# Performance work log

Hardware: AMD Instinct MI355X
Metric: run time of the kernel (lower is better)

## Reference

```python
import jax, jax.numpy as jnp
import numpy as np

N, D_IN = 8192, 1024
FC1, FC2, FC3 = 256, 128, 64
DQK = FC3 // 8  # 8


def setup_inputs() -> dict:
    key = jax.random.key(0)
    ks = jax.random.split(key, 20)
    s = 0.05
    inp = {
        "x": jax.random.normal(ks[0], (N, D_IN), jnp.float32),
        # feature extractor MLP (dropout omitted: eval mode)
        "W1": jax.random.normal(ks[1], (D_IN, FC1), jnp.float32) * s,
        "b1": jnp.zeros((FC1,), jnp.float32),
        "W2": jax.random.normal(ks[2], (FC1, FC2), jnp.float32) * s,
        "b2": jnp.zeros((FC2,), jnp.float32),
        "W3": jax.random.normal(ks[3], (FC2, FC3), jnp.float32) * s,
        "b3": jnp.zeros((FC3,), jnp.float32),
        # 1x1 conv Q/K/V == linear layers on the 64-dim embedding
        "Wq": jax.random.normal(ks[4], (FC3, DQK), jnp.float32) * s,
        "bq": jnp.zeros((DQK,), jnp.float32),
        "Wk": jax.random.normal(ks[5], (FC3, DQK), jnp.float32) * s,
        "bk": jnp.zeros((DQK,), jnp.float32),
        "Wv": jax.random.normal(ks[6], (FC3, FC3), jnp.float32) * s,
        "bv": jnp.zeros((FC3,), jnp.float32),
        "gamma": jnp.array([0.5], jnp.float32),  # learned residual scale (init 0 in torch)
        # attention-pooling branch
        "Wa1": jax.random.normal(ks[7], (FC3, FC3), jnp.float32) * s,
        "ba1": jnp.zeros((FC3,), jnp.float32),
        "Wa2": jax.random.normal(ks[8], (FC3, 1), jnp.float32) * s,
        "ba2": jnp.zeros((1,), jnp.float32),
        # classifier
        "Wc": jax.random.normal(ks[9], (FC3, 1), jnp.float32) * s,
        "bc": jnp.zeros((1,), jnp.float32),
    }
    return inp


def reference(x, W1, b1, W2, b2, W3, b3, Wq, bq, Wk, bk, Wv, bv, gamma,
              Wa1, ba1, Wa2, ba2, Wc, bc):
    # instance feature extractor (dropout identity at eval)
    H = jax.nn.relu(x @ W1 + b1)
    H = jax.nn.relu(H @ W2 + b2)
    H = jax.nn.relu(H @ W3 + b3)                 # [N, 64]
    # self-attention over instances (unscaled dot product)
    Q = H @ Wq + bq                              # [N, 8]
    K = H @ Wk + bk                              # [N, 8]
    V = H @ Wv + bv                              # [N, 64]
    att = jax.nn.softmax(Q @ K.T, axis=-1)       # [N, N] full score matrix
    H = gamma[0] * (att @ V) + H                 # residual scale-add
    # attention-based MIL pooling
    scores = jnp.tanh(H @ Wa1 + ba1) @ Wa2 + ba2 # [N, 1]
    A = jax.nn.softmax(scores[:, 0])             # [N]
    M = A @ H                                    # [64] bag embedding
    Y = jax.nn.sigmoid(M @ Wc + bc)[0]
    Y_prob = jnp.clip(Y, 1e-5, 1.0 - 1e-5)
    return (Y_prob, M)
```

## Files before the change

### kernel.cpp

```cpp
#include <hip/hip_runtime.h>
#include <math.h>

typedef unsigned short ushort_t;
typedef __attribute__((ext_vector_type(8))) short short8;
typedef __attribute__((ext_vector_type(4))) float f32x4;

__device__ inline unsigned bfpair(float lo, float hi) {
  unsigned r;
  asm("v_cvt_pk_bf16_f32 %0, %1, %2" : "=v"(r) : "v"(lo), "v"(hi));
  return r;
}
__device__ inline ushort_t bf16of(float v) { return (ushort_t)(bfpair(v, v) & 0xffffu); }
__device__ inline void permswap32(unsigned &a, unsigned &b) {
  asm("v_permlane32_swap_b32 %0, %1" : "+v"(a), "+v"(b));
}
__device__ inline void permswap16(unsigned &a, unsigned &b) {
  asm("v_permlane16_swap_b32 %0, %1" : "+v"(a), "+v"(b));
}

__device__ void transpose_tile(const float* __restrict__ W, ushort_t* __restrict__ Wt,
                               int K, int N, int bx, int by, int t)
{
  __shared__ float Ls[32][33];
  const int n0 = bx * 32, k0 = by * 32;
  const int tx = t & 31, tyb = t >> 5;
  #pragma unroll
  for (int s = 0; s < 4; ++s) {
    const int k = tyb + s * 8;
    Ls[k][tx] = W[(size_t)(k0 + k) * N + n0 + tx];
  }
  __syncthreads();
  #pragma unroll
  for (int s = 0; s < 2; ++s) {
    const int idx = t + 256 * s;
    const int n = idx >> 4, kk = (idx & 15) * 2;
    const unsigned pk = bfpair(Ls[kk][n], Ls[kk + 1][n]);
    *(unsigned*)&Wt[(size_t)(n0 + n) * K + k0 + kk] = pk;
  }
}

__global__ __launch_bounds__(256) void prep_all_k(
    const float* __restrict__ W1, ushort_t* __restrict__ W1t,
    const float* __restrict__ W2, ushort_t* __restrict__ W2t,
    const float* __restrict__ W3, ushort_t* __restrict__ W3t,
    const float* __restrict__ Wa1, ushort_t* __restrict__ Wa1t,
    const float* __restrict__ Wq, const float* __restrict__ Wk,
    const float* __restrict__ Wv, ushort_t* __restrict__ WqkvT)
{
  const int bid = blockIdx.x;
  const int t = threadIdx.x;
  if (bid < 256)      { transpose_tile(W1, W1t, 1024, 256, bid & 7, bid >> 3, t); }
  else if (bid < 288) { const int l = bid - 256; transpose_tile(W2, W2t, 256, 128, l & 3, l >> 2, t); }
  else if (bid < 296) { const int l = bid - 288; transpose_tile(W3, W3t, 128,  64, l & 1, l >> 1, t); }
  else if (bid < 300) { const int l = bid - 296; transpose_tile(Wa1, Wa1t, 64,  64, l & 1, l >> 1, t); }
  else {
    for (int e = t; e < 80 * 64; e += 256) {
      const int j = e >> 6, k = e & 63;
      float v;
      if (j < 8)       v = Wq[k * 8 + j];
      else if (j < 16) v = Wk[k * 8 + (j - 8)];
      else             v = Wv[k * 64 + (j - 16)];
      WqkvT[e] = bf16of(v);
    }
  }
}

template<int K, int N, int WAVES, bool A_FP32, int OMODE>
__global__ __launch_bounds__(WAVES * 64) void gemm_staged(
    const void* __restrict__ Ap, const ushort_t* __restrict__ Wt,
    const float* __restrict__ bias, void* __restrict__ C0, void* __restrict__ C1)
{
  constexpr int BM = 32;
  constexpr int NWN = N / 32;
  constexpr int NK = K / 32;
  constexpr int A_CH = BM * 4;
  constexpr int B_CH = N * 4;
  static_assert(WAVES * 64 == B_CH, "threads must equal B chunk count");
  static_assert(A_CH <= WAVES * 64, "");

  const int tid = threadIdx.x;
  const int wave = tid >> 6, lane = tid & 63;
  const int ln = lane & 15, g = lane >> 4;
  const int wm = wave / NWN, wn = wave % NWN;
  const int bm0 = blockIdx.x * BM;

  __shared__ ushort_t Als[2][BM][40];
  __shared__ ushort_t Bls[2][N][40];

  const float* Af = (const float*)Ap;
  const ushort_t* Ab = (const ushort_t*)Ap;

  const bool hasA = (tid < A_CH);
  const int arow = tid >> 2, akq = tid & 3;
  const int bc = hasA ? (B_CH - A_CH + tid) : (tid - A_CH);
  const int brow = bc >> 2, bkq = bc & 3;

  float4 rf0, rf1;
  short8 ra, rb;

  auto LOADK = [&](int ks) {
    const int k0 = ks * 32;
    if (hasA) {
      if (A_FP32) {
        const float* src = &Af[(size_t)(bm0 + arow) * K + k0 + akq * 8];
        rf0 = *(const float4*)src;
        rf1 = *(const float4*)(src + 4);
      } else {
        ra = *(const short8*)&Ab[(size_t)(bm0 + arow) * K + k0 + akq * 8];
      }
    }
    rb = *(const short8*)&Wt[(size_t)brow * K + k0 + bkq * 8];
  };
  auto WRITEK = [&](int cur) {
    if (hasA) {
      short8 wa;
      if (A_FP32) {
        union { unsigned u[4]; short8 s8; } cv;
        cv.u[0] = bfpair(rf0.x, rf0.y);
        cv.u[1] = bfpair(rf0.z, rf0.w);
        cv.u[2] = bfpair(rf1.x, rf1.y);
        cv.u[3] = bfpair(rf1.z, rf1.w);
        wa = cv.s8;
      } else {
        wa = ra;
      }
      *(short8*)&Als[cur][arow][akq * 8] = wa;
    }
    *(short8*)&Bls[cur][brow][bkq * 8] = rb;
  };

  f32x4 acc0 = {0.f, 0.f, 0.f, 0.f};
  f32x4 acc1 = {0.f, 0.f, 0.f, 0.f};

  LOADK(0);
  int cur = 0;
  for (int ks = 0; ks < NK; ++ks) {
    WRITEK(cur);
    __syncthreads();
    if (ks + 1 < NK) LOADK(ks + 1);
    const short8 af = *(const short8*)&Als[cur][wm * 16 + ln][g * 8];
    const short8 b0 = *(const short8*)&Bls[cur][wn * 32 + ln][g * 8];
    const short8 b1 = *(const short8*)&Bls[cur][wn * 32 + 16 + ln][g * 8];
    acc0 = __builtin_amdgcn_mfma_f32_16x16x32_bf16(af, b0, acc0, 0, 0, 0);
    acc1 = __builtin_amdgcn_mfma_f32_16x16x32_bf16(af, b1, acc1, 0, 0, 0);
    cur ^= 1;
  }

  #pragma unroll
  for (int nt = 0; nt < 2; ++nt) {
    const f32x4 a = nt ? acc1 : acc0;
    #pragma unroll
    for (int r = 0; r < 4; ++r) {
      const int m = bm0 + wm * 16 + 4 * g + r;
      const int n = wn * 32 + nt * 16 + ln;
      float v = a[r] + bias[n];
      v = fmaxf(v, 0.f);
      if (OMODE == 0) {
        ((ushort_t*)C0)[(size_t)m * N + n] = bf16of(v);
      } else {
        ((float*)C0)[(size_t)m * N + n] = v;
      }
    }
  }
}

__global__ __launch_bounds__(256) void mlp23_qkv_k(
    const ushort_t* __restrict__ H1b, const ushort_t* __restrict__ W2t,
    const float* __restrict__ b2, const ushort_t* __restrict__ W3t,
    const float* __restrict__ b3, const ushort_t* __restrict__ WqkvT,
    const float* __restrict__ bq, const float* __restrict__ bk, const float* __restrict__ bv,
    float* __restrict__ H3, ushort_t* __restrict__ Qb, ushort_t* __restrict__ Kb,
    ushort_t* __restrict__ VT)
{
  const int wave = threadIdx.x >> 6, lane = threadIdx.x & 63;
  const int ln = lane & 15, g = lane >> 4;
  const int q0 = blockIdx.x * 16;
  const f32x4 zero4 = {0.f, 0.f, 0.f, 0.f};

  __shared__ ushort_t H2ls[16][136];
  __shared__ ushort_t Hls[16][72];

  f32x4 a2[2] = {zero4, zero4};
  #pragma unroll 2
  for (int k0 = 0; k0 < 256; k0 += 32) {
    const short8 af = *(const short8*)&H1b[(size_t)(q0 + ln) * 256 + k0 + g * 8];
    const short8 b0 = *(const short8*)&W2t[(size_t)(wave * 32 + ln) * 256 + k0 + g * 8];
    const short8 b1 = *(const short8*)&W2t[(size_t)(wave * 32 + 16 + ln) * 256 + k0 + g * 8];
    a2[0] = __builtin_amdgcn_mfma_f32_16x16x32_bf16(af, b0, a2[0], 0, 0, 0);
    a2[1] = __builtin_amdgcn_mfma_f32_16x16x32_bf16(af, b1, a2[1], 0, 0, 0);
  }
  #pragma unroll
  for (int nt = 0; nt < 2; ++nt)
    #pragma unroll
    for (int r = 0; r < 4; ++r) {
      const int n = wave * 32 + nt * 16 + ln;
      H2ls[4 * g + r][n] = bf16of(fmaxf(a2[nt][r] + b2[n], 0.f));
    }
  __syncthreads();

  f32x4 a3 = zero4;
  #pragma unroll
  for (int k0 = 0; k0 < 128; k0 += 32) {
    const short8 af = *(const short8*)&H2ls[ln][k0 + g * 8];
    const short8 bfr = *(const short8*)&W3t[(size_t)(wave * 16 + ln) * 128 + k0 + g * 8];
    a3 = __builtin_amdgcn_mfma_f32_16x16x32_bf16(af, bfr, a3, 0, 0, 0);
  }
  #pragma unroll
  for (int r = 0; r < 4; ++r) {
    const int m = q0 + 4 * g + r;
    const int n = wave * 16 + ln;
    float v = fmaxf(a3[r] + b3[n], 0.f);
    H3[(size_t)m * 64 + n] = v;
    Hls[4 * g + r][n] = bf16of(v);
  }
  __syncthreads();

  const int ntA = (wave == 0) ? 0 : (wave + 1);
  f32x4 accA = zero4, accB = zero4;
  #pragma unroll
  for (int k0 = 0; k0 < 64; k0 += 32) {
    const short8 af = *(const short8*)&Hls[ln][k0 + g * 8];
    const short8 bA = *(const short8*)&WqkvT[(size_t)(ntA * 16 + ln) * 64 + k0 + g * 8];
    accA = __builtin_amdgcn_mfma_f32_16x16x32_bf16(af, bA, accA, 0, 0, 0);
    if (wave == 0) {
      const short8 bB = *(const short8*)&WqkvT[(size_t)(16 + ln) * 64 + k0 + g * 8];
      accB = __builtin_amdgcn_mfma_f32_16x16x32_bf16(af, bB, accB, 0, 0, 0);
    }
  }
  if (wave == 0) {
    const float b0 = (ln < 8) ? bq[ln] : bk[ln - 8];
    #pragma unroll
    for (int r = 0; r < 4; ++r) {
      const int m = q0 + 4 * g + r;
      const float v = accA[r] + b0;
      if (ln < 8) Qb[(size_t)m * 8 + ln] = bf16of(v);
      else        Kb[(size_t)m * 8 + (ln - 8)] = bf16of(v);
    }
    const int d = ln;
    const float bb = bv[d];
    uint2 o;
    o.x = bfpair(accB[0] + bb, accB[1] + bb);
    o.y = bfpair(accB[2] + bb, accB[3] + bb);
    *(uint2*)&VT[(size_t)d * 8192 + q0 + 4 * g] = o;
  } else {
    const int d = (ntA - 1) * 16 + ln;
    const float bb = bv[d];
    uint2 o;
    o.x = bfpair(accA[0] + bb, accA[1] + bb);
    o.y = bfpair(accA[2] + bb, accA[3] + bb);
    *(uint2*)&VT[(size_t)d * 8192 + q0 + 4 * g] = o;
  }
}

__global__ __launch_bounds__(1024) void attn_part_k(
    const ushort_t* __restrict__ Qb, const ushort_t* __restrict__ Kb,
    const ushort_t* __restrict__ VT, float* __restrict__ Pnum,
    float* __restrict__ Pden)
{
  const int tid = threadIdx.x;
  const int wave = tid >> 6, lane = tid & 63;
  const int m = lane & 15, g = lane >> 4;
  const int qg = blockIdx.x & 31, js = blockIdx.x >> 5;
  const int q0 = qg * 256 + wave * 16;
  const int j0 = js * 1024;
  const f32x4 zero4 = {0.f,0.f,0.f,0.f};

  __shared__ ushort_t Vls[2][64][68];
  __shared__ ushort_t Kls[2][64][12];

  const bool isV = (tid < 512);
  const int vd = tid >> 3, vc = tid & 7;
  const bool isK = (tid >= 512 && tid < 576);
  const int kj = tid - 512;

  short8 vreg = {0,0,0,0,0,0,0,0}, kreg = {0,0,0,0,0,0,0,0};
  auto LOAD = [&](int jb) {
    if (isV) vreg = *(const short8*)&VT[(size_t)vd * 8192 + jb + vc * 8];
    if (isK) kreg = *(const short8*)&Kb[(size_t)(jb + kj) * 8];
  };
  auto WRITE = [&](int cur) {
    if (isV) *(short8*)&Vls[cur][vd][vc * 8] = vreg;
    if (isK) *(short8*)&Kls[cur][kj][0] = kreg;
  };

  short8 qf = {0,0,0,0,0,0,0,0};
  if (lane < 16) qf = *(const short8*)&Qb[(size_t)(q0 + m) * 8];

  f32x4 acc[4];
  #pragma unroll
  for (int dt=0;dt<4;dt++) acc[dt] = zero4;
  float lsum = 0.f;

  LOAD(j0);
  int cur = 0;
  for (int it = 0; it < 16; ++it) {
    WRITE(cur);
    __syncthreads();
    if (it + 1 < 16) LOAD(j0 + (it + 1) * 64);

    #pragma unroll
    for (int half = 0; half < 2; ++half) {
      short8 kf0 = {0,0,0,0,0,0,0,0}, kf1 = {0,0,0,0,0,0,0,0};
      if (lane < 16) {
        kf0 = *(const short8*)&Kls[cur][half*32 + m][0];
        kf1 = *(const short8*)&Kls[cur][half*32 + 16 + m][0];
      }
      const f32x4 s0 = __builtin_amdgcn_mfma_f32_16x16x32_bf16(kf0, qf, zero4, 0,0,0);
      const f32x4 s1 = __builtin_amdgcn_mfma_f32_16x16x32_bf16(kf1, qf, zero4, 0,0,0);
      const float e00 = __expf(s0[0]), e01 = __expf(s0[1]), e02 = __expf(s0[2]), e03 = __expf(s0[3]);
      const float e10 = __expf(s1[0]), e11 = __expf(s1[1]), e12 = __expf(s1[2]), e13 = __expf(s1[3]);
      lsum += ((e00+e01)+(e02+e03)) + ((e10+e11)+(e12+e13));
      unsigned X01 = bfpair(e00,e01), X23 = bfpair(e02,e03);
      unsigned Y01 = bfpair(e10,e11), Y23 = bfpair(e12,e13);
      permswap32(X01, Y01); permswap16(X01, Y01);
      permswap32(X23, Y23); permswap16(X23, Y23);
      union { unsigned u[4]; short8 s; } pfu;
      pfu.u[0] = X01;
      pfu.u[1] = X23;
      pfu.u[2] = Y01;
      pfu.u[3] = Y23;
      #pragma unroll
      for (int dt=0;dt<4;dt++) {
        const short8 vf = *(const short8*)&Vls[cur][dt*16 + m][half*32 + g * 8];
        acc[dt] = __builtin_amdgcn_mfma_f32_16x16x32_bf16(pfu.s, vf, acc[dt], 0,0,0);
      }
    }
    cur ^= 1;
  }

  lsum += __shfl_xor(lsum, 16, 64);
  lsum += __shfl_xor(lsum, 32, 64);

  float* np = &Pnum[((size_t)blockIdx.x * 256 + wave * 16) * 64];
  #pragma unroll
  for (int dt=0;dt<4;dt++)
    #pragma unroll
    for (int r=0;r<4;r++)
      np[(size_t)(4*g + r) * 64 + dt*16 + m] = acc[dt][r];
  if (lane < 16)
    Pden[(size_t)blockIdx.x * 256 + wave * 16 + m] = lsum;
}

__global__ __launch_bounds__(256) void epilogue_k(
    const float* __restrict__ Pnum, const float* __restrict__ Pden,
    const float* __restrict__ H3, const float* __restrict__ gamma,
    const ushort_t* __restrict__ Wa1t, const float* __restrict__ ba1,
    const float* __restrict__ Wa2, const float* __restrict__ ba2,
    float* __restrict__ pM, float* __restrict__ pS)
{
  const int wave = threadIdx.x >> 6, lane = threadIdx.x & 63;
  const int ln = lane & 15, g = lane >> 4;
  const int e = blockIdx.x;
  const int sub = e >> 5, qg = e & 31;
  const int q0 = qg * 256 + sub * 16;
  const f32x4 zero4 = {0.f, 0.f, 0.f, 0.f};

  __shared__ float Hals[16][68];
  __shared__ ushort_t Habls[16][72];
  __shared__ float scls[16];
  __shared__ float Ms[4][64];
  __shared__ float Ss[4];

  const float gm = gamma[0];
  #pragma unroll
  for (int rr = 0; rr < 4; ++rr) {
    const int r = wave * 4 + rr;
    const int q = q0 + r;
    const int qloc = q & 255;
    float num = 0.f, den = 0.f;
    #pragma unroll
    for (int js = 0; js < 8; ++js) {
      const size_t base = (size_t)(js * 32 + qg) * 256 + qloc;
      num += Pnum[base * 64 + lane];
      den += Pden[base];
    }
    const float hv = fmaf(gm, num / den, H3[(size_t)q * 64 + lane]);
    Hals[r][lane] = hv;
    Habls[r][lane] = bf16of(hv);
  }
  __syncthreads();

  f32x4 acc[4];
  #pragma unroll
  for (int nt = 0; nt < 4; ++nt) acc[nt] = zero4;
  #pragma unroll
  for (int k0 = 0; k0 < 64; k0 += 32) {
    const short8 af = *(const short8*)&Habls[ln][k0 + g * 8];
    #pragma unroll
    for (int nt = 0; nt < 4; ++nt) {
      const short8 bfr = *(const short8*)&Wa1t[(size_t)(nt * 16 + ln) * 64 + k0 + g * 8];
      acc[nt] = __builtin_amdgcn_mfma_f32_16x16x32_bf16(af, bfr, acc[nt], 0, 0, 0);
    }
  }
  #pragma unroll
  for (int r = 0; r < 4; ++r) {
    float s = 0.f;
    #pragma unroll
    for (int nt = 0; nt < 4; ++nt) {
      const int n = nt * 16 + ln;
      s += tanhf(acc[nt][r] + ba1[n]) * Wa2[n];
    }
    s += __shfl_xor(s, 1, 64); s += __shfl_xor(s, 2, 64);
    s += __shfl_xor(s, 4, 64); s += __shfl_xor(s, 8, 64);
    if (ln == 0) scls[4 * g + r] = s + ba2[0];
  }
  float macc = 0.f, se = 0.f;
  #pragma unroll
  for (int rr = 0; rr < 4; ++rr) {
    const int r = wave * 4 + rr;
    const float ee = __expf(scls[r]);
    se += ee;
    macc = fmaf(ee, Hals[r][lane], macc);
  }
  Ms[wave][lane] = macc;
  if (lane == 0) Ss[wave] = se;
  __syncthreads();
  if (wave == 0) {
    pM[(size_t)e * 64 + lane] = Ms[0][lane] + Ms[1][lane] + Ms[2][lane] + Ms[3][lane];
    if (lane == 0) pS[e] = Ss[0] + Ss[1] + Ss[2] + Ss[3];
  }
}

__global__ __launch_bounds__(1024) void pool2_k(
    const float* __restrict__ pM, const float* __restrict__ pS,
    const float* __restrict__ Wc, const float* __restrict__ bc,
    float* __restrict__ out)
{
  const int wave = threadIdx.x >> 6, lane = threadIdx.x & 63;
  __shared__ float Ms2[16][64];
  __shared__ float Ss2[16];
  float m_ = 0.f;
  #pragma unroll
  for (int i = 0; i < 32; ++i)
    m_ += pM[(size_t)(wave * 32 + i) * 64 + lane];
  Ms2[wave][lane] = m_;
  float s_ = (lane < 32) ? pS[wave * 32 + lane] : 0.f;
  s_ += __shfl_xor(s_, 1, 64);  s_ += __shfl_xor(s_, 2, 64);
  s_ += __shfl_xor(s_, 4, 64);  s_ += __shfl_xor(s_, 8, 64);
  s_ += __shfl_xor(s_, 16, 64); s_ += __shfl_xor(s_, 32, 64);
  if (lane == 0) Ss2[wave] = s_;
  __syncthreads();
  if (wave == 0) {
    float mm = 0.f, ss = 0.f;
    #pragma unroll
    for (int i = 0; i < 16; ++i) { mm += Ms2[i][lane]; ss += Ss2[i]; }
    const float Md = mm / ss;
    out[1 + lane] = Md;
    float yp = Md * Wc[lane];
    yp += __shfl_xor(yp, 1, 64);  yp += __shfl_xor(yp, 2, 64);
    yp += __shfl_xor(yp, 4, 64);  yp += __shfl_xor(yp, 8, 64);
    yp += __shfl_xor(yp, 16, 64); yp += __shfl_xor(yp, 32, 64);
    if (lane == 0) {
      float y = 1.f / (1.f + __expf(-(yp + bc[0])));
      y = fminf(fmaxf(y, 1e-5f), 1.f - 1e-5f);
      out[0] = y;
    }
  }
}

extern "C" void kernel_launch(void* const* d_in, const int* in_sizes, int n_in,
                              void* d_out, int out_size, void* d_ws, size_t ws_size,
                              hipStream_t stream)
{
  const float* x    = (const float*)d_in[0];
  const float* W1   = (const float*)d_in[1];
  const float* b1   = (const float*)d_in[2];
  const float* W2   = (const float*)d_in[3];
  const float* b2   = (const float*)d_in[4];
  const float* W3   = (const float*)d_in[5];
  const float* b3   = (const float*)d_in[6];
  const float* Wq   = (const float*)d_in[7];
  const float* bq   = (const float*)d_in[8];
  const float* Wk   = (const float*)d_in[9];
  const float* bk   = (const float*)d_in[10];
  const float* Wv   = (const float*)d_in[11];
  const float* bv   = (const float*)d_in[12];
  const float* gam  = (const float*)d_in[13];
  const float* Wa1  = (const float*)d_in[14];
  const float* ba1  = (const float*)d_in[15];
  const float* Wa2  = (const float*)d_in[16];
  const float* ba2  = (const float*)d_in[17];
  const float* Wc   = (const float*)d_in[18];
  const float* bc   = (const float*)d_in[19];
  float* out = (float*)d_out;

  char* w = (char*)d_ws;
  float* H3 = (float*)w;        w += (size_t)8192*64*4;
  float* pM = (float*)w;        w += 512*64*4;
  float* pS = (float*)w;        w += 512*4;
  float* Pnum = (float*)w;      w += (size_t)256*256*64*4;
  float* Pden = (float*)w;      w += (size_t)256*256*4;
  ushort_t* H1b = (ushort_t*)w; w += (size_t)8192*256*2;
  ushort_t* Qb  = (ushort_t*)w; w += (size_t)8192*8*2;
  ushort_t* Kb  = (ushort_t*)w; w += (size_t)8192*8*2;
  ushort_t* VT  = (ushort_t*)w; w += (size_t)64*8192*2;
  ushort_t* W1t = (ushort_t*)w; w += (size_t)256*1024*2;
  ushort_t* W2t = (ushort_t*)w; w += (size_t)128*256*2;
  ushort_t* W3t = (ushort_t*)w; w += (size_t)64*128*2;
  ushort_t* Wa1t= (ushort_t*)w; w += (size_t)64*64*2;
  ushort_t* Wqkv= (ushort_t*)w; w += (size_t)80*64*2;

  prep_all_k<<<301, 256, 0, stream>>>(W1, W1t, W2, W2t, W3, W3t, Wa1, Wa1t,
                                      Wq, Wk, Wv, Wqkv);
  gemm_staged<1024,256,16,true ,0><<<256, 1024, 0, stream>>>(x, W1t, b1, H1b, nullptr);
  mlp23_qkv_k<<<512, 256, 0, stream>>>(H1b, W2t, b2, W3t, b3, Wqkv,
                                       bq, bk, bv, H3, Qb, Kb, VT);
  attn_part_k<<<256, 1024, 0, stream>>>(Qb, Kb, VT, Pnum, Pden);
  epilogue_k<<<512, 256, 0, stream>>>(Pnum, Pden, H3, gam, Wa1t, ba1, Wa2, ba2, pM, pS);
  pool2_k<<<1, 1024, 0, stream>>>(pM, pS, Wc, bc, out);
}
```

Baseline: 77.80 us.

## Give each attention wave two query tiles and split keys across more blocks

The attention partial kernel now runs 512-thread blocks in which each wave handles 32 queries (two 16-row MFMA tiles), so every K/V fragment read from LDS feeds two query tiles. The key range per block is halved to 512, which doubles the grid to 512 blocks and doubles the number of partial results. The aim is fewer LDS reads and fewer syncs per unit of work, plus more blocks to fill the CUs. The cost is twice as many partial numerator/denominator writes and reads, since the epilogue now reduces 16 partials instead of 8, along with more accumulator registers per thread.

```diff
diff --git a/kernel.cpp b/kernel.cpp
--- a/kernel.cpp
+++ b/kernel.cpp
@@ -252,7 +252,7 @@
   }
 }
 
-__global__ __launch_bounds__(1024) void attn_part_k(
+__global__ __launch_bounds__(512) void attn_part_k(
     const ushort_t* __restrict__ Qb, const ushort_t* __restrict__ Kb,
     const ushort_t* __restrict__ VT, float* __restrict__ Pnum,
     float* __restrict__ Pden)
@@ -261,42 +261,45 @@
   const int wave = tid >> 6, lane = tid & 63;
   const int m = lane & 15, g = lane >> 4;
   const int qg = blockIdx.x & 31, js = blockIdx.x >> 5;
-  const int q0 = qg * 256 + wave * 16;
-  const int j0 = js * 1024;
+  const int q0 = qg * 256 + wave * 32;
+  const int j0 = js * 512;
   const f32x4 zero4 = {0.f,0.f,0.f,0.f};
 
   __shared__ ushort_t Vls[2][64][68];
   __shared__ ushort_t Kls[2][64][12];
 
-  const bool isV = (tid < 512);
   const int vd = tid >> 3, vc = tid & 7;
-  const bool isK = (tid >= 512 && tid < 576);
-  const int kj = tid - 512;
+  const bool isK = (tid < 64);
 
   short8 vreg = {0,0,0,0,0,0,0,0}, kreg = {0,0,0,0,0,0,0,0};
   auto LOAD = [&](int jb) {
-    if (isV) vreg = *(const short8*)&VT[(size_t)vd * 8192 + jb + vc * 8];
-    if (isK) kreg = *(const short8*)&Kb[(size_t)(jb + kj) * 8];
+    vreg = *(const short8*)&VT[(size_t)vd * 8192 + jb + vc * 8];
+    if (isK) kreg = *(const short8*)&Kb[(size_t)(jb + tid) * 8];
   };
   auto WRITE = [&](int cur) {
-    if (isV) *(short8*)&Vls[cur][vd][vc * 8] = vreg;
-    if (isK) *(short8*)&Kls[cur][kj][0] = kreg;
+    *(short8*)&Vls[cur][vd][vc * 8] = vreg;
+    if (isK) *(short8*)&Kls[cur][tid][0] = kreg;
   };
 
-  short8 qf = {0,0,0,0,0,0,0,0};
-  if (lane < 16) qf = *(const short8*)&Qb[(size_t)(q0 + m) * 8];
-
-  f32x4 acc[4];
-  #pragma unroll
-  for (int dt=0;dt<4;dt++) acc[dt] = zero4;
-  float lsum = 0.f;
+  short8 qf[2] = {{0,0,0,0,0,0,0,0},{0,0,0,0,0,0,0,0}};
+  if (lane < 16) {
+    qf[0] = *(const short8*)&Qb[(size_t)(q0 + m) * 8];
+    qf[1] = *(const short8*)&Qb[(size_t)(q0 + 16 + m) * 8];
+  }
+
+  f32x4 acc[2][4];
+  #pragma unroll
+  for (int qt=0;qt<2;qt++)
+    #pragma unroll
+    for (int dt=0;dt<4;dt++) acc[qt][dt] = zero4;
+  float lsum[2] = {0.f, 0.f};
 
   LOAD(j0);
   int cur = 0;
-  for (int it = 0; it < 16; ++it) {
+  for (int it = 0; it < 8; ++it) {
     WRITE(cur);
     __syncthreads();
-    if (it + 1 < 16) LOAD(j0 + (it + 1) * 64);
+    if (it + 1 < 8) LOAD(j0 + (it + 1) * 64);
 
     #pragma unroll
     for (int half = 0; half < 2; ++half) {
@@ -305,40 +308,53 @@
         kf0 = *(const short8*)&Kls[cur][half*32 + m][0];
         kf1 = *(const short8*)&Kls[cur][half*32 + 16 + m][0];
       }
-      const f32x4 s0 = __builtin_amdgcn_mfma_f32_16x16x32_bf16(kf0, qf, zero4, 0,0,0);
-      const f32x4 s1 = __builtin_amdgcn_mfma_f32_16x16x32_bf16(kf1, qf, zero4, 0,0,0);
-      const float e00 = __expf(s0[0]), e01 = __expf(s0[1]), e02 = __expf(s0[2]), e03 = __expf(s0[3]);
-      const float e10 = __expf(s1[0]), e11 = __expf(s1[1]), e12 = __expf(s1[2]), e13 = __expf(s1[3]);
-      lsum += ((e00+e01)+(e02+e03)) + ((e10+e11)+(e12+e13));
-      unsigned X01 = bfpair(e00,e01), X23 = bfpair(e02,e03);
-      unsigned Y01 = bfpair(e10,e11), Y23 = bfpair(e12,e13);
-      permswap32(X01, Y01); permswap16(X01, Y01);
-      permswap32(X23, Y23); permswap16(X23, Y23);
-      union { unsigned u[4]; short8 s; } pfu;
-      pfu.u[0] = X01;
-      pfu.u[1] = X23;
-      pfu.u[2] = Y01;
-      pfu.u[3] = Y23;
+      short8 pf[2];
+      #pragma unroll
+      for (int qt = 0; qt < 2; ++qt) {
+        const f32x4 s0 = __builtin_amdgcn_mfma_f32_16x16x32_bf16(kf0, qf[qt], zero4, 0,0,0);
+        const f32x4 s1 = __builtin_amdgcn_mfma_f32_16x16x32_bf16(kf1, qf[qt], zero4, 0,0,0);
+        const float e00 = __expf(s0[0]), e01 = __expf(s0[1]), e02 = __expf(s0[2]), e03 = __expf(s0[3]);
+        const float e10 = __expf(s1[0]), e11 = __expf(s1[1]), e12 = __expf(s1[2]), e13 = __expf(s1[3]);
+        lsum[qt] += ((e00+e01)+(e02+e03)) + ((e10+e11)+(e12+e13));
+        unsigned X01 = bfpair(e00,e01), X23 = bfpair(e02,e03);
+        unsigned Y01 = bfpair(e10,e11), Y23 = bfpair(e12,e13);
+        permswap32(X01, Y01); permswap16(X01, Y01);
+        permswap32(X23, Y23); permswap16(X23, Y23);
+        union { unsigned u[4]; short8 s; } pfu;
+        pfu.u[0] = X01;
+        pfu.u[1] = X23;
+        pfu.u[2] = Y01;
+        pfu.u[3] = Y23;
+        pf[qt] = pfu.s;
+      }
       #pragma unroll
       for (int dt=0;dt<4;dt++) {
         const short8 vf = *(const short8*)&Vls[cur][dt*16 + m][half*32 + g * 8];
-        acc[dt] = __builtin_amdgcn_mfma_f32_16x16x32_bf16(pfu.s, vf, acc[dt], 0,0,0);
+        acc[0][dt] = __builtin_amdgcn_mfma_f32_16x16x32_bf16(pf[0], vf, acc[0][dt], 0,0,0);
+        acc[1][dt] = __builtin_amdgcn_mfma_f32_16x16x32_bf16(pf[1], vf, acc[1][dt], 0,0,0);
       }
     }
     cur ^= 1;
   }
 
-  lsum += __shfl_xor(lsum, 16, 64);
-  lsum += __shfl_xor(lsum, 32, 64);
-
-  float* np = &Pnum[((size_t)blockIdx.x * 256 + wave * 16) * 64];
-  #pragma unroll
-  for (int dt=0;dt<4;dt++)
-    #pragma unroll
-    for (int r=0;r<4;r++)
-      np[(size_t)(4*g + r) * 64 + dt*16 + m] = acc[dt][r];
-  if (lane < 16)
-    Pden[(size_t)blockIdx.x * 256 + wave * 16 + m] = lsum;
+  #pragma unroll
+  for (int qt=0;qt<2;qt++) {
+    lsum[qt] += __shfl_xor(lsum[qt], 16, 64);
+    lsum[qt] += __shfl_xor(lsum[qt], 32, 64);
+  }
+
+  float* np = &Pnum[((size_t)blockIdx.x * 256 + wave * 32) * 64];
+  #pragma unroll
+  for (int qt=0;qt<2;qt++)
+    #pragma unroll
+    for (int dt=0;dt<4;dt++)
+      #pragma unroll
+      for (int r=0;r<4;r++)
+        np[(size_t)(qt*16 + 4*g + r) * 64 + dt*16 + m] = acc[qt][dt][r];
+  if (lane < 16) {
+    Pden[(size_t)blockIdx.x * 256 + wave * 32 + m] = lsum[0];
+    Pden[(size_t)blockIdx.x * 256 + wave * 32 + 16 + m] = lsum[1];
+  }
 }
 
 __global__ __launch_bounds__(256) void epilogue_k(
@@ -369,7 +385,7 @@
     const int qloc = q & 255;
     float num = 0.f, den = 0.f;
     #pragma unroll
-    for (int js = 0; js < 8; ++js) {
+    for (int js = 0; js < 16; ++js) {
       const size_t base = (size_t)(js * 32 + qg) * 256 + qloc;
       num += Pnum[base * 64 + lane];
       den += Pden[base];
@@ -488,8 +504,8 @@
   float* H3 = (float*)w;        w += (size_t)8192*64*4;
   float* pM = (float*)w;        w += 512*64*4;
   float* pS = (float*)w;        w += 512*4;
-  float* Pnum = (float*)w;      w += (size_t)256*256*64*4;
-  float* Pden = (float*)w;      w += (size_t)256*256*4;
+  float* Pnum = (float*)w;      w += (size_t)512*256*64*4;
+  float* Pden = (float*)w;      w += (size_t)512*256*4;
   ushort_t* H1b = (ushort_t*)w; w += (size_t)8192*256*2;
   ushort_t* Qb  = (ushort_t*)w; w += (size_t)8192*8*2;
   ushort_t* Kb  = (ushort_t*)w; w += (size_t)8192*8*2;
@@ -505,7 +521,7 @@
   gemm_staged<1024,256,16,true ,0><<<256, 1024, 0, stream>>>(x, W1t, b1, H1b, nullptr);
   mlp23_qkv_k<<<512, 256, 0, stream>>>(H1b, W2t, b2, W3t, b3, Wqkv,
                                        bq, bk, bv, H3, Qb, Kb, VT);
-  attn_part_k<<<256, 1024, 0, stream>>>(Qb, Kb, VT, Pnum, Pden);
+  attn_part_k<<<512, 512, 0, stream>>>(Qb, Kb, VT, Pnum, Pden);
   epilogue_k<<<512, 256, 0, stream>>>(Pnum, Pden, H3, gam, Wa1t, ba1, Wa2, ba2, pM, pS);
   pool2_k<<<1, 1024, 0, stream>>>(pM, pS, Wc, bc, out);
 }
```

New measurement: 102.6 us. 1.32x slower.
